# Optimization experiments

Measured on AMD Instinct MI355X. Metric: run time of the kernel, lower is better.

The kernel has to match this reference:

```python
import jax, jax.numpy as jnp
import numpy as np

B, V, NB, NJ, NEXTRA = 512, 6890, 10, 24, 9
PARENTS = np.array([-1,0,0,0,1,2,3,4,5,6,7,8,9,9,9,12,13,14,16,17,18,19,20,21], dtype=np.int32)


def setup_inputs() -> dict:
    key = jax.random.key(0)
    ks = jax.random.split(key, 11)
    betas = jax.random.normal(ks[0], (B, NB + 1), jnp.float32) * 0.1
    betas = betas.at[:, 0].set(1.0)  # col 0 is a global scale in this SMPL variant
    body_pose = jax.random.normal(ks[1], (B, 3 * (NJ - 1)), jnp.float32) * 0.2
    global_orient = jax.random.normal(ks[2], (B, 3), jnp.float32) * 0.2
    transl = jax.random.normal(ks[3], (B, 3), jnp.float32) * 0.1
    model_scale_opt = jnp.ones((1,), jnp.float32)
    smpl_v_template = jax.random.normal(ks[4], (V, 3), jnp.float32)
    smil_v_template = jax.random.normal(ks[5], (V, 3), jnp.float32)
    shapedirs = jax.random.normal(ks[6], (V, 3, NB), jnp.float32) * 0.01
    J_regressor = jax.nn.softmax(jax.random.normal(ks[7], (NJ, V), jnp.float32), axis=1)
    lbs_weights = jax.nn.softmax(jax.random.normal(ks[8], (V, NJ), jnp.float32) * 4.0, axis=1)
    J_regressor_extra = jax.nn.softmax(jax.random.normal(ks[9], (NEXTRA, V), jnp.float32), axis=1)
    parents = jnp.asarray(PARENTS)
    return dict(betas=betas, body_pose=body_pose, global_orient=global_orient,
                transl=transl, model_scale_opt=model_scale_opt,
                smpl_v_template=smpl_v_template, smil_v_template=smil_v_template,
                shapedirs=shapedirs, J_regressor=J_regressor, lbs_weights=lbs_weights,
                J_regressor_extra=J_regressor_extra, parents=parents)


def batch_rodrigues(rvecs):
    # rvecs: [N,3] axis-angle -> [N,3,3] rotation matrices
    angle = jnp.linalg.norm(rvecs + 1e-8, axis=1, keepdims=True)  # [N,1]
    axis = rvecs / angle
    c = jnp.cos(angle)[..., None]  # [N,1,1]
    s = jnp.sin(angle)[..., None]
    rx, ry, rz = axis[:, 0], axis[:, 1], axis[:, 2]
    z = jnp.zeros_like(rx)
    K = jnp.stack([z, -rz, ry, rz, z, -rx, -ry, rx, z], axis=1).reshape(-1, 3, 3)
    I = jnp.eye(3, dtype=rvecs.dtype)
    return I + s * K + (1.0 - c) * jnp.matmul(K, K)


def _smpl_forward(betas, body_pose, global_orient, transl, model_scale_opt,
                  smpl_v_template, smil_v_template, shapedirs,
                  J_regressor, lbs_weights, J_regressor_extra):
    dtype = betas.dtype
    # ---- updateShape ----
    s = model_scale_opt[0]
    v_template = smpl_v_template * s + (1.0 - s) * smil_v_template  # [V,3]
    blend_shape = jnp.einsum('bl,mkl->bmk', betas[:, 1:], shapedirs)  # [B,V,3]
    v_shaped = (v_template[None] + blend_shape) * betas[:, :1, None]  # scale col
    J_shaped = jnp.einsum('bik,ji->bjk', v_shaped, J_regressor)  # [B,NJ,3]

    # ---- updatePose ----
    full_pose = jnp.concatenate([global_orient, body_pose], axis=1)  # [B,NJ*3]
    rot_mats = batch_rodrigues(full_pose.reshape(-1, 3)).reshape(B, NJ, 3, 3)

    # relative joint locations w.r.t. parents
    rel_joints = J_shaped.at[:, 1:].add(-J_shaped[:, PARENTS[1:]])
    top = jnp.concatenate([rot_mats, rel_joints[..., None]], axis=-1)  # [B,NJ,3,4]
    bottom = jnp.broadcast_to(
        jnp.array([0.0, 0.0, 0.0, 1.0], dtype=dtype), (B, NJ, 1, 4))
    mats = jnp.concatenate([top, bottom], axis=2)  # [B,NJ,4,4]

    # sequential kinematic-chain composition over the 24-joint tree
    chain = [mats[:, 0]]
    for i in range(1, NJ):
        chain.append(jnp.matmul(chain[PARENTS[i]], mats[:, i]))
    chain = jnp.stack(chain, axis=1)  # [B,NJ,4,4]
    posed_joints = chain[:, :, :3, 3]  # [B,NJ,3]

    # relative transforms: subtract rotated rest joints
    corr = jnp.einsum('bjmn,bjn->bjm', chain[:, :, :3, :3], J_shaped)
    A = chain.at[:, :, :3, 3].add(-corr)  # [B,NJ,4,4]

    # linear blend skinning
    T = jnp.einsum('vj,bjmn->bvmn', lbs_weights, A)  # [B,V,4,4]
    verts = jnp.einsum('bvmn,bvn->bvm', T[:, :, :3, :3], v_shaped) + T[:, :, :3, 3]

    extra_joints = jnp.einsum('bik,ji->bjk', verts, J_regressor_extra)  # [B,9,3]
    joints = jnp.concatenate([posed_joints, extra_joints], axis=1)  # [B,33,3]

    t = transl[:, None, :]
    # concat verts and joints along point dim for a single output array
    return jnp.concatenate([verts + t, joints + t], axis=1)  # [B, V+33, 3]


def reference(betas, body_pose, global_orient, transl, model_scale_opt,
              smpl_v_template, smil_v_template, shapedirs,
              J_regressor, lbs_weights, J_regressor_extra, parents):
    return _smpl_forward(betas, body_pose, global_orient, transl, model_scale_opt,
                         smpl_v_template, smil_v_template, shapedirs,
                         J_regressor, lbs_weights, J_regressor_extra)
```

## Files before the change

### kernel.cpp

```cpp
#include <hip/hip_runtime.h>


#define BATCH 512
#define NV 6890
#define NBD 10
#define NJ 24
#define NEXTRA 9
#define NOUT (NV + NJ + NEXTRA)
#define VBLK ((NV + 255) / 256)
#define BPB 4

__constant__ int c_par[NJ] = {-1,0,0,0,1,2,3,4,5,6,7,8,9,9,9,12,13,14,16,17,18,19,20,21};

__global__ __launch_bounds__(256) void precompute_kernel(
    const float* __restrict__ jreg,
    const float* __restrict__ smpl_t,
    const float* __restrict__ smil_t,
    const float* __restrict__ sdirs,
    const float* __restrict__ msc,
    float* __restrict__ jtjs)
{
    const int j = blockIdx.y;
    const int v = blockIdx.x * 256 + threadIdx.x;
    const float s = msc[0];

    float acc[33];
#pragma unroll
    for (int i = 0; i < 33; ++i) acc[i] = 0.f;

    if (v < NV) {
        const float w = jreg[j * NV + v];
#pragma unroll
        for (int k = 0; k < 3; ++k) {
            float vt = s * smpl_t[v * 3 + k] + (1.f - s) * smil_t[v * 3 + k];
            acc[k] = w * vt;
        }
        const float2* sd2 = (const float2*)(sdirs + (size_t)v * 30);
#pragma unroll
        for (int i = 0; i < 15; ++i) {
            float2 x = sd2[i];
            acc[3 + 2 * i]     = w * x.x;
            acc[3 + 2 * i + 1] = w * x.y;
        }
    }

#pragma unroll
    for (int i = 0; i < 33; ++i) {
        float x = acc[i];
        for (int off = 32; off; off >>= 1) x += __shfl_xor(x, off, 64);
        acc[i] = x;
    }

    __shared__ float red[4][33];
    const int lane = threadIdx.x & 63, wv = threadIdx.x >> 6;
    if (lane == 0) {
#pragma unroll
        for (int i = 0; i < 33; ++i) red[wv][i] = acc[i];
    }
    __syncthreads();
    if (threadIdx.x < 33) {
        float sum = red[0][threadIdx.x] + red[1][threadIdx.x]
                  + red[2][threadIdx.x] + red[3][threadIdx.x];
        atomicAdd(&jtjs[j * 33 + threadIdx.x], sum);
    }
}

__global__ __launch_bounds__(64) void joints_kernel(
    const float* __restrict__ betas,
    const float* __restrict__ body_pose,
    const float* __restrict__ glob_or,
    const float* __restrict__ transl,
    const float* __restrict__ jtjs,
    float* __restrict__ wsA,
    float* __restrict__ out)
{
    const int b = blockIdx.x;
    const int j = threadIdx.x;

    __shared__ float sJ[NJ][3];
    __shared__ float mats[NJ][12];
    __shared__ float chain[NJ][12];
    __shared__ float sbeta[NBD + 1];

    if (threadIdx.x < NBD + 1) sbeta[threadIdx.x] = betas[b * (NBD + 1) + threadIdx.x];
    __syncthreads();

    if (j < NJ) {
        const float beta0 = sbeta[0];
#pragma unroll
        for (int k = 0; k < 3; ++k) {
            float a = jtjs[j * 33 + k];
#pragma unroll
            for (int l = 0; l < NBD; ++l) a = fmaf(sbeta[1 + l], jtjs[j * 33 + 3 + k * 10 + l], a);
            sJ[j][k] = a * beta0;
        }
        float rx, ry, rz;
        if (j == 0) {
            rx = glob_or[b * 3 + 0]; ry = glob_or[b * 3 + 1]; rz = glob_or[b * 3 + 2];
        } else {
            rx = body_pose[b * 69 + (j - 1) * 3 + 0];
            ry = body_pose[b * 69 + (j - 1) * 3 + 1];
            rz = body_pose[b * 69 + (j - 1) * 3 + 2];
        }
        float ex = rx + 1e-8f, ey = ry + 1e-8f, ez = rz + 1e-8f;
        float ang = sqrtf(ex * ex + ey * ey + ez * ez);
        float inv = 1.f / ang;
        float ax = rx * inv, ay = ry * inv, az = rz * inv;
        float c = cosf(ang), s = sinf(ang), t = 1.f - c;
        mats[j][0]  = 1.f + t * (-(ay * ay + az * az));
        mats[j][1]  = -s * az + t * (ax * ay);
        mats[j][2]  =  s * ay + t * (ax * az);
        mats[j][4]  =  s * az + t * (ax * ay);
        mats[j][5]  = 1.f + t * (-(ax * ax + az * az));
        mats[j][6]  = -s * ax + t * (ay * az);
        mats[j][8]  = -s * ay + t * (ax * az);
        mats[j][9]  =  s * ax + t * (ay * az);
        mats[j][10] = 1.f + t * (-(ax * ax + ay * ay));
    }
    __syncthreads();
    if (j < NJ) {
        const int p = c_par[j];
        float t0 = sJ[j][0], t1 = sJ[j][1], t2 = sJ[j][2];
        if (p >= 0) { t0 -= sJ[p][0]; t1 -= sJ[p][1]; t2 -= sJ[p][2]; }
        mats[j][3] = t0; mats[j][7] = t1; mats[j][11] = t2;
    }
    __syncthreads();
    if (threadIdx.x == 0) {
#pragma unroll
        for (int k = 0; k < 12; ++k) chain[0][k] = mats[0][k];
        for (int i = 1; i < NJ; ++i) {
            const int p = c_par[i];
#pragma unroll
            for (int r = 0; r < 3; ++r) {
#pragma unroll
                for (int col = 0; col < 4; ++col) {
                    float acc = (col == 3) ? chain[p][r * 4 + 3] : 0.f;
#pragma unroll
                    for (int q = 0; q < 3; ++q) acc = fmaf(chain[p][r * 4 + q], mats[i][q * 4 + col], acc);
                    chain[i][r * 4 + col] = acc;
                }
            }
        }
    }
    __syncthreads();
    if (j < NJ) {
        float A[12];
#pragma unroll
        for (int k = 0; k < 12; ++k) A[k] = chain[j][k];
        const float c0 = A[3], c1 = A[7], c2 = A[11];
        const float j0 = sJ[j][0], j1 = sJ[j][1], j2 = sJ[j][2];
        A[3]  = c0 - (A[0] * j0 + A[1] * j1 + A[2]  * j2);
        A[7]  = c1 - (A[4] * j0 + A[5] * j1 + A[6]  * j2);
        A[11] = c2 - (A[8] * j0 + A[9] * j1 + A[10] * j2);
#pragma unroll
        for (int k = 0; k < 12; ++k) wsA[((size_t)b * NJ + j) * 12 + k] = A[k];
        const float tx = transl[b * 3 + 0], ty = transl[b * 3 + 1], tz = transl[b * 3 + 2];
        const size_t o = ((size_t)b * NOUT + NV + j) * 3;
        out[o + 0] = c0 + tx; out[o + 1] = c1 + ty; out[o + 2] = c2 + tz;
    }
}

__global__ __launch_bounds__(256) void lbs_kernel(
    const float* __restrict__ betas,
    const float* __restrict__ transl,
    const float* __restrict__ msc,
    const float* __restrict__ smpl_t,
    const float* __restrict__ smil_t,
    const float* __restrict__ sdirs,
    const float* __restrict__ lbsw,
    const float* __restrict__ wsA,
    float* __restrict__ out)
{
    const int v = blockIdx.x * 256 + threadIdx.x;
    const bool valid = v < NV;
    const int vc = valid ? v : NV - 1;
    const int b0 = blockIdx.y * BPB;
    const float s = msc[0];

    float vt[3];
#pragma unroll
    for (int k = 0; k < 3; ++k)
        vt[k] = s * smpl_t[vc * 3 + k] + (1.f - s) * smil_t[vc * 3 + k];

    float sd[30];
    {
        const float2* sd2 = (const float2*)(sdirs + (size_t)vc * 30);
#pragma unroll
        for (int i = 0; i < 15; ++i) { float2 x = sd2[i]; sd[2 * i] = x.x; sd[2 * i + 1] = x.y; }
    }
    float w[NJ];
    {
        const float4* w4 = (const float4*)(lbsw + (size_t)vc * NJ);
#pragma unroll
        for (int i = 0; i < 6; ++i) {
            float4 x = w4[i];
            w[4 * i] = x.x; w[4 * i + 1] = x.y; w[4 * i + 2] = x.z; w[4 * i + 3] = x.w;
        }
    }

#pragma unroll
    for (int bb = 0; bb < BPB; ++bb) {
        const int b = b0 + bb;
        const float* __restrict__ Bb = betas + b * (NBD + 1);
        const float* __restrict__ Ab = wsA + (size_t)b * NJ * 12;

        float vs[3];
#pragma unroll
        for (int k = 0; k < 3; ++k) {
            float a = vt[k];
#pragma unroll
            for (int l = 0; l < NBD; ++l) a = fmaf(Bb[1 + l], sd[k * 10 + l], a);
            vs[k] = a * Bb[0];
        }

        float T[12];
#pragma unroll
        for (int k = 0; k < 12; ++k) T[k] = 0.f;
#pragma unroll 4
        for (int jj = 0; jj < NJ; ++jj) {
            const float ww = w[jj];
#pragma unroll
            for (int k = 0; k < 12; ++k) T[k] = fmaf(ww, Ab[jj * 12 + k], T[k]);
        }

        if (valid) {
            const float tx = transl[b * 3 + 0], ty = transl[b * 3 + 1], tz = transl[b * 3 + 2];
            const size_t o = ((size_t)b * NOUT + v) * 3;
            out[o + 0] = fmaf(T[0], vs[0], fmaf(T[1], vs[1], fmaf(T[2],  vs[2], T[3])))  + tx;
            out[o + 1] = fmaf(T[4], vs[0], fmaf(T[5], vs[1], fmaf(T[6],  vs[2], T[7])))  + ty;
            out[o + 2] = fmaf(T[8], vs[0], fmaf(T[9], vs[1], fmaf(T[10], vs[2], T[11]))) + tz;
        }
    }
}

__global__ __launch_bounds__(256) void extra_kernel(
    const float* __restrict__ jre,
    float* out)
{
    const int b = blockIdx.x;
    const float* vb = out + (size_t)b * NOUT * 3;

    float acc[27];
#pragma unroll
    for (int i = 0; i < 27; ++i) acc[i] = 0.f;

    for (int v = threadIdx.x; v < NV; v += 256) {
        const float x = vb[v * 3 + 0], y = vb[v * 3 + 1], z = vb[v * 3 + 2];
#pragma unroll
        for (int e = 0; e < NEXTRA; ++e) {
            const float we = jre[e * NV + v];
            acc[e * 3 + 0] = fmaf(we, x, acc[e * 3 + 0]);
            acc[e * 3 + 1] = fmaf(we, y, acc[e * 3 + 1]);
            acc[e * 3 + 2] = fmaf(we, z, acc[e * 3 + 2]);
        }
    }

#pragma unroll
    for (int i = 0; i < 27; ++i) {
        float x = acc[i];
        for (int off = 32; off; off >>= 1) x += __shfl_xor(x, off, 64);
        acc[i] = x;
    }
    __shared__ float red[4][27];
    const int lane = threadIdx.x & 63, wv = threadIdx.x >> 6;
    if (lane == 0) {
#pragma unroll
        for (int i = 0; i < 27; ++i) red[wv][i] = acc[i];
    }
    __syncthreads();
    if (threadIdx.x < 27) {
        const float sum = red[0][threadIdx.x] + red[1][threadIdx.x]
                        + red[2][threadIdx.x] + red[3][threadIdx.x];
        out[((size_t)b * NOUT + NV + NJ) * 3 + threadIdx.x] = sum;
    }
}

extern "C" void kernel_launch(void* const* d_in, const int* in_sizes, int n_in,
                              void* d_out, int out_size, void* d_ws, size_t ws_size,
                              hipStream_t stream) {
    const float* betas     = (const float*)d_in[0];
    const float* body_pose = (const float*)d_in[1];
    const float* glob_or   = (const float*)d_in[2];
    const float* transl    = (const float*)d_in[3];
    const float* msc       = (const float*)d_in[4];
    const float* smpl_t    = (const float*)d_in[5];
    const float* smil_t    = (const float*)d_in[6];
    const float* sdirs     = (const float*)d_in[7];
    const float* jreg      = (const float*)d_in[8];
    const float* lbsw      = (const float*)d_in[9];
    const float* jre       = (const float*)d_in[10];

    float* out  = (float*)d_out;
    float* ws   = (float*)d_ws;
    float* jtjs = ws;
    float* wsA  = ws + 792;

    hipMemsetAsync(jtjs, 0, NJ * 33 * sizeof(float), stream);

    dim3 gA(VBLK, NJ);
    precompute_kernel<<<gA, 256, 0, stream>>>(jreg, smpl_t, smil_t, sdirs, msc, jtjs);

    joints_kernel<<<BATCH, 64, 0, stream>>>(betas, body_pose, glob_or, transl, jtjs, wsA, out);

    dim3 gC(VBLK, BATCH / BPB);
    lbs_kernel<<<gC, 256, 0, stream>>>(betas, transl, msc, smpl_t, smil_t, sdirs, lbsw, wsA, out);

    extra_kernel<<<BATCH, 256, 0, stream>>>(jre, out);
}
```

Baseline: 186.3 us.

## Parallelize kinematic chain by level, 2 verts per thread in LBS, split extra reduction

The joints kernel now composes the kinematic chain level by level, with one thread per joint, instead of running it serially on thread 0. The LBS kernel gives each thread two vertices so every joint-transform load is reused across both. The extra-joint regression is split into four vertex chunks per batch, with a small finalize kernel summing the partials. This raises parallelism and data reuse, at the cost of more registers per LBS thread and an extra kernel launch.

Result: slower. 218.1 us (+17.1%).

```diff
diff --git a/kernel.cpp b/kernel.cpp
--- a/kernel.cpp
+++ b/kernel.cpp
@@ -9,8 +9,13 @@
 #define NOUT (NV + NJ + NEXTRA)
 #define VBLK ((NV + 255) / 256)
 #define BPB 4
+#define VPT 2
+#define VB (256 * VPT)
+#define NCHUNK 4
+#define CHUNKV ((NV + NCHUNK - 1) / NCHUNK)
 
 __constant__ int c_par[NJ] = {-1,0,0,0,1,2,3,4,5,6,7,8,9,9,9,12,13,14,16,17,18,19,20,21};
+__constant__ int c_lvl[NJ] = { 0,1,1,1,2,2,2,3,3,3,4,4,4, 4, 4, 5, 5, 5, 6, 6, 7, 7, 8, 8};
 
 __global__ __launch_bounds__(256) void precompute_kernel(
     const float* __restrict__ jreg,
@@ -78,13 +83,13 @@
     const int j = threadIdx.x;
 
     __shared__ float sJ[NJ][3];
-    __shared__ float mats[NJ][12];
     __shared__ float chain[NJ][12];
     __shared__ float sbeta[NBD + 1];
 
     if (threadIdx.x < NBD + 1) sbeta[threadIdx.x] = betas[b * (NBD + 1) + threadIdx.x];
     __syncthreads();
 
+    float M[12];
     if (j < NJ) {
         const float beta0 = sbeta[0];
 #pragma unroll
@@ -107,42 +112,51 @@
         float inv = 1.f / ang;
         float ax = rx * inv, ay = ry * inv, az = rz * inv;
         float c = cosf(ang), s = sinf(ang), t = 1.f - c;
-        mats[j][0]  = 1.f + t * (-(ay * ay + az * az));
-        mats[j][1]  = -s * az + t * (ax * ay);
-        mats[j][2]  =  s * ay + t * (ax * az);
-        mats[j][4]  =  s * az + t * (ax * ay);
-        mats[j][5]  = 1.f + t * (-(ax * ax + az * az));
-        mats[j][6]  = -s * ax + t * (ay * az);
-        mats[j][8]  = -s * ay + t * (ax * az);
-        mats[j][9]  =  s * ax + t * (ay * az);
-        mats[j][10] = 1.f + t * (-(ax * ax + ay * ay));
+        M[0]  = 1.f + t * (-(ay * ay + az * az));
+        M[1]  = -s * az + t * (ax * ay);
+        M[2]  =  s * ay + t * (ax * az);
+        M[4]  =  s * az + t * (ax * ay);
+        M[5]  = 1.f + t * (-(ax * ax + az * az));
+        M[6]  = -s * ax + t * (ay * az);
+        M[8]  = -s * ay + t * (ax * az);
+        M[9]  =  s * ax + t * (ay * az);
+        M[10] = 1.f + t * (-(ax * ax + ay * ay));
     }
     __syncthreads();
     if (j < NJ) {
         const int p = c_par[j];
         float t0 = sJ[j][0], t1 = sJ[j][1], t2 = sJ[j][2];
         if (p >= 0) { t0 -= sJ[p][0]; t1 -= sJ[p][1]; t2 -= sJ[p][2]; }
-        mats[j][3] = t0; mats[j][7] = t1; mats[j][11] = t2;
-    }
-    __syncthreads();
-    if (threadIdx.x == 0) {
-#pragma unroll
-        for (int k = 0; k < 12; ++k) chain[0][k] = mats[0][k];
-        for (int i = 1; i < NJ; ++i) {
-            const int p = c_par[i];
+        M[3] = t0; M[7] = t1; M[11] = t2;
+        if (j == 0) {
+#pragma unroll
+            for (int k = 0; k < 12; ++k) chain[0][k] = M[k];
+        }
+    }
+    __syncthreads();
+#pragma unroll
+    for (int level = 1; level <= 8; ++level) {
+        if (j < NJ && c_lvl[j] == level) {
+            const int p = c_par[j];
+            float P[12];
+#pragma unroll
+            for (int k = 0; k < 12; ++k) P[k] = chain[p][k];
+            float C[12];
 #pragma unroll
             for (int r = 0; r < 3; ++r) {
 #pragma unroll
                 for (int col = 0; col < 4; ++col) {
-                    float acc = (col == 3) ? chain[p][r * 4 + 3] : 0.f;
-#pragma unroll
-                    for (int q = 0; q < 3; ++q) acc = fmaf(chain[p][r * 4 + q], mats[i][q * 4 + col], acc);
-                    chain[i][r * 4 + col] = acc;
+                    float acc = (col == 3) ? P[r * 4 + 3] : 0.f;
+#pragma unroll
+                    for (int q = 0; q < 3; ++q) acc = fmaf(P[r * 4 + q], M[q * 4 + col], acc);
+                    C[r * 4 + col] = acc;
                 }
             }
-        }
-    }
-    __syncthreads();
+#pragma unroll
+            for (int k = 0; k < 12; ++k) chain[j][k] = C[k];
+        }
+        __syncthreads();
+    }
     if (j < NJ) {
         float A[12];
 #pragma unroll
@@ -171,30 +185,39 @@
     const float* __restrict__ wsA,
     float* __restrict__ out)
 {
-    const int v = blockIdx.x * 256 + threadIdx.x;
-    const bool valid = v < NV;
-    const int vc = valid ? v : NV - 1;
+    const int vbase = blockIdx.x * VB + threadIdx.x;
     const int b0 = blockIdx.y * BPB;
     const float s = msc[0];
 
-    float vt[3];
-#pragma unroll
-    for (int k = 0; k < 3; ++k)
-        vt[k] = s * smpl_t[vc * 3 + k] + (1.f - s) * smil_t[vc * 3 + k];
-
-    float sd[30];
-    {
+    int   vidx[VPT];
+    bool  valid[VPT];
+#pragma unroll
+    for (int u = 0; u < VPT; ++u) {
+        int v = vbase + u * 256;
+        valid[u] = v < NV;
+        vidx[u] = valid[u] ? v : NV - 1;
+    }
+
+    float vt[VPT][3];
+    float sd[VPT][30];
+    float w[VPT][NJ];
+#pragma unroll
+    for (int u = 0; u < VPT; ++u) {
+        const int vc = vidx[u];
+#pragma unroll
+        for (int k = 0; k < 3; ++k)
+            vt[u][k] = s * smpl_t[vc * 3 + k] + (1.f - s) * smil_t[vc * 3 + k];
         const float2* sd2 = (const float2*)(sdirs + (size_t)vc * 30);
 #pragma unroll
-        for (int i = 0; i < 15; ++i) { float2 x = sd2[i]; sd[2 * i] = x.x; sd[2 * i + 1] = x.y; }
-    }
-    float w[NJ];
-    {
+        for (int i = 0; i < 15; ++i) {
+            float2 x = sd2[i];
+            sd[u][2 * i] = x.x; sd[u][2 * i + 1] = x.y;
+        }
         const float4* w4 = (const float4*)(lbsw + (size_t)vc * NJ);
 #pragma unroll
         for (int i = 0; i < 6; ++i) {
             float4 x = w4[i];
-            w[4 * i] = x.x; w[4 * i + 1] = x.y; w[4 * i + 2] = x.z; w[4 * i + 3] = x.w;
+            w[u][4 * i] = x.x; w[u][4 * i + 1] = x.y; w[u][4 * i + 2] = x.z; w[u][4 * i + 3] = x.w;
         }
     }
 
@@ -204,47 +227,66 @@
         const float* __restrict__ Bb = betas + b * (NBD + 1);
         const float* __restrict__ Ab = wsA + (size_t)b * NJ * 12;
 
-        float vs[3];
-#pragma unroll
-        for (int k = 0; k < 3; ++k) {
-            float a = vt[k];
-#pragma unroll
-            for (int l = 0; l < NBD; ++l) a = fmaf(Bb[1 + l], sd[k * 10 + l], a);
-            vs[k] = a * Bb[0];
-        }
-
-        float T[12];
-#pragma unroll
-        for (int k = 0; k < 12; ++k) T[k] = 0.f;
+        float vs[VPT][3];
+#pragma unroll
+        for (int u = 0; u < VPT; ++u) {
+#pragma unroll
+            for (int k = 0; k < 3; ++k) {
+                float a = vt[u][k];
+#pragma unroll
+                for (int l = 0; l < NBD; ++l) a = fmaf(Bb[1 + l], sd[u][k * 10 + l], a);
+                vs[u][k] = a * Bb[0];
+            }
+        }
+
+        float T[VPT][12];
+#pragma unroll
+        for (int u = 0; u < VPT; ++u)
+#pragma unroll
+            for (int k = 0; k < 12; ++k) T[u][k] = 0.f;
+
 #pragma unroll 4
         for (int jj = 0; jj < NJ; ++jj) {
-            const float ww = w[jj];
-#pragma unroll
-            for (int k = 0; k < 12; ++k) T[k] = fmaf(ww, Ab[jj * 12 + k], T[k]);
-        }
-
-        if (valid) {
-            const float tx = transl[b * 3 + 0], ty = transl[b * 3 + 1], tz = transl[b * 3 + 2];
-            const size_t o = ((size_t)b * NOUT + v) * 3;
-            out[o + 0] = fmaf(T[0], vs[0], fmaf(T[1], vs[1], fmaf(T[2],  vs[2], T[3])))  + tx;
-            out[o + 1] = fmaf(T[4], vs[0], fmaf(T[5], vs[1], fmaf(T[6],  vs[2], T[7])))  + ty;
-            out[o + 2] = fmaf(T[8], vs[0], fmaf(T[9], vs[1], fmaf(T[10], vs[2], T[11]))) + tz;
+            float a[12];
+#pragma unroll
+            for (int k = 0; k < 12; ++k) a[k] = Ab[jj * 12 + k];
+#pragma unroll
+            for (int u = 0; u < VPT; ++u) {
+                const float ww = w[u][jj];
+#pragma unroll
+                for (int k = 0; k < 12; ++k) T[u][k] = fmaf(ww, a[k], T[u][k]);
+            }
+        }
+
+        const float tx = transl[b * 3 + 0], ty = transl[b * 3 + 1], tz = transl[b * 3 + 2];
+#pragma unroll
+        for (int u = 0; u < VPT; ++u) {
+            if (valid[u]) {
+                const size_t o = ((size_t)b * NOUT + vidx[u]) * 3;
+                out[o + 0] = fmaf(T[u][0], vs[u][0], fmaf(T[u][1], vs[u][1], fmaf(T[u][2],  vs[u][2], T[u][3])))  + tx;
+                out[o + 1] = fmaf(T[u][4], vs[u][0], fmaf(T[u][5], vs[u][1], fmaf(T[u][6],  vs[u][2], T[u][7])))  + ty;
+                out[o + 2] = fmaf(T[u][8], vs[u][0], fmaf(T[u][9], vs[u][1], fmaf(T[u][10], vs[u][2], T[u][11]))) + tz;
+            }
         }
     }
 }
 
 __global__ __launch_bounds__(256) void extra_kernel(
     const float* __restrict__ jre,
-    float* out)
+    const float* __restrict__ out,
+    float* __restrict__ part)
 {
     const int b = blockIdx.x;
+    const int c = blockIdx.y;
+    const int v0 = c * CHUNKV;
+    const int v1 = min(NV, v0 + CHUNKV);
     const float* vb = out + (size_t)b * NOUT * 3;
 
     float acc[27];
 #pragma unroll
     for (int i = 0; i < 27; ++i) acc[i] = 0.f;
 
-    for (int v = threadIdx.x; v < NV; v += 256) {
+    for (int v = v0 + threadIdx.x; v < v1; v += 256) {
         const float x = vb[v * 3 + 0], y = vb[v * 3 + 1], z = vb[v * 3 + 2];
 #pragma unroll
         for (int e = 0; e < NEXTRA; ++e) {
@@ -269,9 +311,22 @@
     }
     __syncthreads();
     if (threadIdx.x < 27) {
-        const float sum = red[0][threadIdx.x] + red[1][threadIdx.x]
-                        + red[2][threadIdx.x] + red[3][threadIdx.x];
-        out[((size_t)b * NOUT + NV + NJ) * 3 + threadIdx.x] = sum;
+        part[((size_t)b * NCHUNK + c) * 27 + threadIdx.x] =
+            red[0][threadIdx.x] + red[1][threadIdx.x] + red[2][threadIdx.x] + red[3][threadIdx.x];
+    }
+}
+
+__global__ __launch_bounds__(256) void extra_fin_kernel(
+    const float* __restrict__ part,
+    float* __restrict__ out)
+{
+    const int idx = blockIdx.x * 256 + threadIdx.x;
+    if (idx < BATCH * 27) {
+        const int b = idx / 27, i = idx % 27;
+        float sum = 0.f;
+#pragma unroll
+        for (int c = 0; c < NCHUNK; ++c) sum += part[((size_t)b * NCHUNK + c) * 27 + i];
+        out[((size_t)b * NOUT + NV + NJ) * 3 + i] = sum;
     }
 }
 
@@ -294,6 +349,7 @@
     float* ws   = (float*)d_ws;
     float* jtjs = ws;
     float* wsA  = ws + 792;
+    float* part = wsA + (size_t)BATCH * NJ * 12;
 
     hipMemsetAsync(jtjs, 0, NJ * 33 * sizeof(float), stream);
 
@@ -302,8 +358,11 @@
 
     joints_kernel<<<BATCH, 64, 0, stream>>>(betas, body_pose, glob_or, transl, jtjs, wsA, out);
 
-    dim3 gC(VBLK, BATCH / BPB);
+    dim3 gC((NV + VB - 1) / VB, BATCH / BPB);
     lbs_kernel<<<gC, 256, 0, stream>>>(betas, transl, msc, smpl_t, smil_t, sdirs, lbsw, wsA, out);
 
-    extra_kernel<<<BATCH, 256, 0, stream>>>(jre, out);
-}
+    dim3 gD(BATCH, NCHUNK);
+    extra_kernel<<<gD, 256, 0, stream>>>(jre, out, part);
+
+    extra_fin_kernel<<<(BATCH * 27 + 255) / 256, 256, 0, stream>>>(part, out);
+}
```

## Fuse extra-joint regression into LBS kernel and parallelize kinematic chain by level

Applied to the files above, without the earlier changes.

Removes the separate extra_kernel. The LBS kernel now multiplies each posed vertex by the extra-joint regressor weights, reduces the products across the wavefront with shuffles, and adds them to the output with atomics; joints_kernel zero-initialises that output region first. This avoids re-reading all vertices from global memory, at the cost of many atomics and 27 shuffle reductions per batch element. The joints kernel also replaces the serial single-thread chain walk with a level-by-level, shuffle-based parallel composition, and the LBS kernel stages the A matrices in LDS and fully unrolls the joint loop, adding launch bounds of 4.

Measured after the change: 666.0 us. 257% more time.

```diff
diff --git a/kernel.cpp b/kernel.cpp
--- a/kernel.cpp
+++ b/kernel.cpp
@@ -11,6 +11,7 @@
 #define BPB 4
 
 __constant__ int c_par[NJ] = {-1,0,0,0,1,2,3,4,5,6,7,8,9,9,9,12,13,14,16,17,18,19,20,21};
+__constant__ int c_lvl[NJ] = { 0,1,1,1,2,2,2,3,3,3,4,4,4, 4, 4, 5, 5, 5, 6, 6, 7, 7, 8, 8};
 
 __global__ __launch_bounds__(256) void precompute_kernel(
     const float* __restrict__ jreg,
@@ -76,24 +77,28 @@
 {
     const int b = blockIdx.x;
     const int j = threadIdx.x;
-
-    __shared__ float sJ[NJ][3];
-    __shared__ float mats[NJ][12];
-    __shared__ float chain[NJ][12];
-    __shared__ float sbeta[NBD + 1];
-
-    if (threadIdx.x < NBD + 1) sbeta[threadIdx.x] = betas[b * (NBD + 1) + threadIdx.x];
-    __syncthreads();
-
-    if (j < NJ) {
-        const float beta0 = sbeta[0];
-#pragma unroll
-        for (int k = 0; k < 3; ++k) {
-            float a = jtjs[j * 33 + k];
-#pragma unroll
-            for (int l = 0; l < NBD; ++l) a = fmaf(sbeta[1 + l], jtjs[j * 33 + 3 + k * 10 + l], a);
-            sJ[j][k] = a * beta0;
-        }
+    const bool act = j < NJ;
+
+    const float beta0 = betas[b * (NBD + 1)];
+
+    float sJ0 = 0.f, sJ1 = 0.f, sJ2 = 0.f;
+    float M[12];
+#pragma unroll
+    for (int k = 0; k < 12; ++k) M[k] = 0.f;
+
+    if (act) {
+        float a0 = jtjs[j * 33 + 0];
+        float a1 = jtjs[j * 33 + 1];
+        float a2 = jtjs[j * 33 + 2];
+#pragma unroll
+        for (int l = 0; l < NBD; ++l) {
+            const float bl = betas[b * (NBD + 1) + 1 + l];
+            a0 = fmaf(bl, jtjs[j * 33 + 3 + 0 * 10 + l], a0);
+            a1 = fmaf(bl, jtjs[j * 33 + 3 + 1 * 10 + l], a1);
+            a2 = fmaf(bl, jtjs[j * 33 + 3 + 2 * 10 + l], a2);
+        }
+        sJ0 = a0 * beta0; sJ1 = a1 * beta0; sJ2 = a2 * beta0;
+
         float rx, ry, rz;
         if (j == 0) {
             rx = glob_or[b * 3 + 0]; ry = glob_or[b * 3 + 1]; rz = glob_or[b * 3 + 2];
@@ -107,60 +112,73 @@
         float inv = 1.f / ang;
         float ax = rx * inv, ay = ry * inv, az = rz * inv;
         float c = cosf(ang), s = sinf(ang), t = 1.f - c;
-        mats[j][0]  = 1.f + t * (-(ay * ay + az * az));
-        mats[j][1]  = -s * az + t * (ax * ay);
-        mats[j][2]  =  s * ay + t * (ax * az);
-        mats[j][4]  =  s * az + t * (ax * ay);
-        mats[j][5]  = 1.f + t * (-(ax * ax + az * az));
-        mats[j][6]  = -s * ax + t * (ay * az);
-        mats[j][8]  = -s * ay + t * (ax * az);
-        mats[j][9]  =  s * ax + t * (ay * az);
-        mats[j][10] = 1.f + t * (-(ax * ax + ay * ay));
-    }
-    __syncthreads();
-    if (j < NJ) {
-        const int p = c_par[j];
-        float t0 = sJ[j][0], t1 = sJ[j][1], t2 = sJ[j][2];
-        if (p >= 0) { t0 -= sJ[p][0]; t1 -= sJ[p][1]; t2 -= sJ[p][2]; }
-        mats[j][3] = t0; mats[j][7] = t1; mats[j][11] = t2;
-    }
-    __syncthreads();
-    if (threadIdx.x == 0) {
-#pragma unroll
-        for (int k = 0; k < 12; ++k) chain[0][k] = mats[0][k];
-        for (int i = 1; i < NJ; ++i) {
-            const int p = c_par[i];
+        M[0]  = 1.f + t * (-(ay * ay + az * az));
+        M[1]  = -s * az + t * (ax * ay);
+        M[2]  =  s * ay + t * (ax * az);
+        M[4]  =  s * az + t * (ax * ay);
+        M[5]  = 1.f + t * (-(ax * ax + az * az));
+        M[6]  = -s * ax + t * (ay * az);
+        M[8]  = -s * ay + t * (ax * az);
+        M[9]  =  s * ax + t * (ay * az);
+        M[10] = 1.f + t * (-(ax * ax + ay * ay));
+    }
+
+    const int p = act ? c_par[j] : 0;
+    const int psel = (p >= 0) ? p : 0;
+    const int lvl = act ? c_lvl[j] : 0;
+
+    {
+        float pj0 = __shfl(sJ0, psel);
+        float pj1 = __shfl(sJ1, psel);
+        float pj2 = __shfl(sJ2, psel);
+        if (act) {
+            M[3]  = sJ0 - ((p >= 0) ? pj0 : 0.f);
+            M[7]  = sJ1 - ((p >= 0) ? pj1 : 0.f);
+            M[11] = sJ2 - ((p >= 0) ? pj2 : 0.f);
+        }
+    }
+
+    float C[12];
+#pragma unroll
+    for (int k = 0; k < 12; ++k) C[k] = M[k];
+#pragma unroll
+    for (int level = 1; level <= 8; ++level) {
+        float P[12];
+#pragma unroll
+        for (int k = 0; k < 12; ++k) P[k] = __shfl(C[k], psel);
+        if (act && lvl == level) {
 #pragma unroll
             for (int r = 0; r < 3; ++r) {
 #pragma unroll
                 for (int col = 0; col < 4; ++col) {
-                    float acc = (col == 3) ? chain[p][r * 4 + 3] : 0.f;
-#pragma unroll
-                    for (int q = 0; q < 3; ++q) acc = fmaf(chain[p][r * 4 + q], mats[i][q * 4 + col], acc);
-                    chain[i][r * 4 + col] = acc;
+                    float acc = (col == 3) ? P[r * 4 + 3] : 0.f;
+#pragma unroll
+                    for (int q = 0; q < 3; ++q)
+                        acc = fmaf(P[r * 4 + q], M[q * 4 + col], acc);
+                    C[r * 4 + col] = acc;
                 }
             }
         }
     }
-    __syncthreads();
-    if (j < NJ) {
-        float A[12];
-#pragma unroll
-        for (int k = 0; k < 12; ++k) A[k] = chain[j][k];
-        const float c0 = A[3], c1 = A[7], c2 = A[11];
-        const float j0 = sJ[j][0], j1 = sJ[j][1], j2 = sJ[j][2];
-        A[3]  = c0 - (A[0] * j0 + A[1] * j1 + A[2]  * j2);
-        A[7]  = c1 - (A[4] * j0 + A[5] * j1 + A[6]  * j2);
-        A[11] = c2 - (A[8] * j0 + A[9] * j1 + A[10] * j2);
-#pragma unroll
-        for (int k = 0; k < 12; ++k) wsA[((size_t)b * NJ + j) * 12 + k] = A[k];
+
+    if (act) {
+        const float c0 = C[3], c1 = C[7], c2 = C[11];
+        float A3  = c0 - (C[0] * sJ0 + C[1] * sJ1 + C[2]  * sJ2);
+        float A7  = c1 - (C[4] * sJ0 + C[5] * sJ1 + C[6]  * sJ2);
+        float A11 = c2 - (C[8] * sJ0 + C[9] * sJ1 + C[10] * sJ2);
+        float* Aout = wsA + ((size_t)b * NJ + j) * 12;
+        Aout[0] = C[0]; Aout[1] = C[1]; Aout[2]  = C[2];  Aout[3]  = A3;
+        Aout[4] = C[4]; Aout[5] = C[5]; Aout[6]  = C[6];  Aout[7]  = A7;
+        Aout[8] = C[8]; Aout[9] = C[9]; Aout[10] = C[10]; Aout[11] = A11;
+
         const float tx = transl[b * 3 + 0], ty = transl[b * 3 + 1], tz = transl[b * 3 + 2];
         const size_t o = ((size_t)b * NOUT + NV + j) * 3;
         out[o + 0] = c0 + tx; out[o + 1] = c1 + ty; out[o + 2] = c2 + tz;
     }
+    if (j < 27) out[((size_t)b * NOUT + NV + NJ) * 3 + j] = 0.f;
 }
 
-__global__ __launch_bounds__(256) void lbs_kernel(
+__global__ __launch_bounds__(256, 4) void lbs_kernel(
     const float* __restrict__ betas,
     const float* __restrict__ transl,
     const float* __restrict__ msc,
@@ -168,15 +186,22 @@
     const float* __restrict__ smil_t,
     const float* __restrict__ sdirs,
     const float* __restrict__ lbsw,
+    const float* __restrict__ jre,
     const float* __restrict__ wsA,
     float* __restrict__ out)
 {
-    const int v = blockIdx.x * 256 + threadIdx.x;
+    __shared__ float sA[BPB * NJ * 12];
+
+    const int tid = threadIdx.x;
+    const int v = blockIdx.x * 256 + tid;
     const bool valid = v < NV;
     const int vc = valid ? v : NV - 1;
     const int b0 = blockIdx.y * BPB;
     const float s = msc[0];
 
+    for (int i = tid; i < BPB * NJ * 12; i += 256)
+        sA[i] = wsA[(size_t)b0 * NJ * 12 + i];
+
     float vt[3];
 #pragma unroll
     for (int k = 0; k < 3; ++k)
@@ -197,12 +222,18 @@
             w[4 * i] = x.x; w[4 * i + 1] = x.y; w[4 * i + 2] = x.z; w[4 * i + 3] = x.w;
         }
     }
-
-#pragma unroll
+    float je[NEXTRA];
+#pragma unroll
+    for (int e = 0; e < NEXTRA; ++e)
+        je[e] = valid ? jre[e * NV + vc] : 0.f;
+
+    __syncthreads();
+
+#pragma unroll 1
     for (int bb = 0; bb < BPB; ++bb) {
         const int b = b0 + bb;
         const float* __restrict__ Bb = betas + b * (NBD + 1);
-        const float* __restrict__ Ab = wsA + (size_t)b * NJ * 12;
+        const float* Ab = sA + bb * NJ * 12;
 
         float vs[3];
 #pragma unroll
@@ -216,62 +247,41 @@
         float T[12];
 #pragma unroll
         for (int k = 0; k < 12; ++k) T[k] = 0.f;
-#pragma unroll 4
+#pragma unroll
         for (int jj = 0; jj < NJ; ++jj) {
             const float ww = w[jj];
 #pragma unroll
             for (int k = 0; k < 12; ++k) T[k] = fmaf(ww, Ab[jj * 12 + k], T[k]);
         }
 
+        const float tx = transl[b * 3 + 0], ty = transl[b * 3 + 1], tz = transl[b * 3 + 2];
+        const float ox = fmaf(T[0], vs[0], fmaf(T[1], vs[1], fmaf(T[2],  vs[2], T[3])))  + tx;
+        const float oy = fmaf(T[4], vs[0], fmaf(T[5], vs[1], fmaf(T[6],  vs[2], T[7])))  + ty;
+        const float oz = fmaf(T[8], vs[0], fmaf(T[9], vs[1], fmaf(T[10], vs[2], T[11]))) + tz;
+
         if (valid) {
-            const float tx = transl[b * 3 + 0], ty = transl[b * 3 + 1], tz = transl[b * 3 + 2];
             const size_t o = ((size_t)b * NOUT + v) * 3;
-            out[o + 0] = fmaf(T[0], vs[0], fmaf(T[1], vs[1], fmaf(T[2],  vs[2], T[3])))  + tx;
-            out[o + 1] = fmaf(T[4], vs[0], fmaf(T[5], vs[1], fmaf(T[6],  vs[2], T[7])))  + ty;
-            out[o + 2] = fmaf(T[8], vs[0], fmaf(T[9], vs[1], fmaf(T[10], vs[2], T[11]))) + tz;
-        }
-    }
-}
-
-__global__ __launch_bounds__(256) void extra_kernel(
-    const float* __restrict__ jre,
-    float* out)
-{
-    const int b = blockIdx.x;
-    const float* vb = out + (size_t)b * NOUT * 3;
-
-    float acc[27];
-#pragma unroll
-    for (int i = 0; i < 27; ++i) acc[i] = 0.f;
-
-    for (int v = threadIdx.x; v < NV; v += 256) {
-        const float x = vb[v * 3 + 0], y = vb[v * 3 + 1], z = vb[v * 3 + 2];
+            out[o + 0] = ox; out[o + 1] = oy; out[o + 2] = oz;
+        }
+
+        float acc[27];
 #pragma unroll
         for (int e = 0; e < NEXTRA; ++e) {
-            const float we = jre[e * NV + v];
-            acc[e * 3 + 0] = fmaf(we, x, acc[e * 3 + 0]);
-            acc[e * 3 + 1] = fmaf(we, y, acc[e * 3 + 1]);
-            acc[e * 3 + 2] = fmaf(we, z, acc[e * 3 + 2]);
-        }
-    }
-
-#pragma unroll
-    for (int i = 0; i < 27; ++i) {
-        float x = acc[i];
-        for (int off = 32; off; off >>= 1) x += __shfl_xor(x, off, 64);
-        acc[i] = x;
-    }
-    __shared__ float red[4][27];
-    const int lane = threadIdx.x & 63, wv = threadIdx.x >> 6;
-    if (lane == 0) {
-#pragma unroll
-        for (int i = 0; i < 27; ++i) red[wv][i] = acc[i];
-    }
-    __syncthreads();
-    if (threadIdx.x < 27) {
-        const float sum = red[0][threadIdx.x] + red[1][threadIdx.x]
-                        + red[2][threadIdx.x] + red[3][threadIdx.x];
-        out[((size_t)b * NOUT + NV + NJ) * 3 + threadIdx.x] = sum;
+            acc[e * 3 + 0] = je[e] * ox;
+            acc[e * 3 + 1] = je[e] * oy;
+            acc[e * 3 + 2] = je[e] * oz;
+        }
+#pragma unroll
+        for (int i = 0; i < 27; ++i) {
+            float x = acc[i];
+            for (int off = 32; off; off >>= 1) x += __shfl_xor(x, off, 64);
+            acc[i] = x;
+        }
+        if ((tid & 63) == 0) {
+            float* dst = out + ((size_t)b * NOUT + NV + NJ) * 3;
+#pragma unroll
+            for (int i = 0; i < 27; ++i) atomicAdd(&dst[i], acc[i]);
+        }
     }
 }
 
@@ -303,7 +313,6 @@
     joints_kernel<<<BATCH, 64, 0, stream>>>(betas, body_pose, glob_or, transl, jtjs, wsA, out);
 
     dim3 gC(VBLK, BATCH / BPB);
-    lbs_kernel<<<gC, 256, 0, stream>>>(betas, transl, msc, smpl_t, smil_t, sdirs, lbsw, wsA, out);
-
-    extra_kernel<<<BATCH, 256, 0, stream>>>(jre, out);
+    lbs_kernel<<<gC, 256, 0, stream>>>(betas, transl, msc, smpl_t, smil_t, sdirs,
+                                       lbsw, jre, wsA, out);
 }
```
